# Optimization experiments

Hardware: AMD Instinct MI355X
Metric: run time of the kernel (lower is better)

Reference implementation:

```python
import jax, jax.numpy as jnp
import numpy as np

D = 12  # grid size per axis (self.shape = [12,12,12])
BN_EPS = 1e-5


def _scatter(feats, idx, B):
    # feats: [N, C], idx: [N, 4] = (b, z, y, x). Coords are unique -> .set is exact.
    g = jnp.zeros((B, D, D, D, feats.shape[-1]), feats.dtype)
    return g.at[idx[:, 0], idx[:, 1], idx[:, 2], idx[:, 3]].set(feats)


def _subm_conv_bn_relu(feats, idx, B, W, b, gamma, beta):
    # Submanifold 3x3x3 conv == dense SAME conv on zero-filled grid, restricted
    # to the active sites (inactive neighbors contribute zero features).
    g = _scatter(feats, idx, B)  # [B, D, D, D, Cin]
    y = jax.lax.conv_general_dilated(
        g, W, window_strides=(1, 1, 1), padding='SAME',
        dimension_numbers=('NDHWC', 'DHWIO', 'NDHWC')) + b
    f = y[idx[:, 0], idx[:, 1], idx[:, 2], idx[:, 3]]  # gather active -> [N, Cout]
    # BatchNorm1d (training mode): biased batch stats over the N active points.
    mu = f.mean(axis=0)
    var = f.var(axis=0)
    f = (f - mu) * jax.lax.rsqrt(var + BN_EPS) * gamma + beta
    return jax.nn.relu(f)


def setup_inputs() -> dict:
    key = jax.random.key(0)
    B, per, Cin = 512, 864, 16
    N = B * per
    k_feat, k_coord, kp = jax.random.split(key, 3)
    # unique active voxels per batch element
    pkeys = jax.random.split(k_coord, B)
    lin = jax.vmap(lambda k: jax.random.permutation(k, D * D * D))(pkeys)[:, :per]  # [B, per]
    z, y, x = lin // (D * D), (lin // D) % D, lin % D
    bids = jnp.broadcast_to(jnp.arange(B)[:, None], (B, per))
    indices = jnp.stack([bids, z, y, x], axis=-1).reshape(N, 4).astype(jnp.int32)
    features = jax.random.normal(k_feat, (N, Cin), dtype=jnp.float32)
    ks = jax.random.split(kp, 6)
    inp = {
        'features': features, 'indices': indices, 'batch_size': B,
        'W0': jax.random.normal(ks[0], (3, 3, 3, Cin, 64), jnp.float32) * 0.05,
        'b0': jax.random.normal(ks[1], (64,), jnp.float32) * 0.05,
        'gamma0': jnp.ones((64,), jnp.float32), 'beta0': jnp.zeros((64,), jnp.float32),
        'W1': jax.random.normal(ks[2], (3, 3, 3, 64, 128), jnp.float32) * 0.05,
        'b1': jax.random.normal(ks[3], (128,), jnp.float32) * 0.05,
        'gamma1': jnp.ones((128,), jnp.float32), 'beta1': jnp.zeros((128,), jnp.float32),
        'W2': jax.random.normal(ks[4], (3, 3, 3, 128, 64), jnp.float32) * 0.05,
        'b2': jax.random.normal(ks[5], (64,), jnp.float32) * 0.05,
        'gamma2': jnp.ones((64,), jnp.float32), 'beta2': jnp.zeros((64,), jnp.float32),
    }
    return inp


def reference(features, indices, batch_size, W0, b0, gamma0, beta0,
              W1, b1, gamma1, beta1, W2, b2, gamma2, beta2):
    B = int(batch_size)
    f = _subm_conv_bn_relu(features, indices, B, W0, b0, gamma0, beta0)
    f = _subm_conv_bn_relu(f, indices, B, W1, b1, gamma1, beta1)
    f = _subm_conv_bn_relu(f, indices, B, W2, b2, gamma2, beta2)
    g = _scatter(f, indices, B)                 # [B, D, D, D, Cout]
    return jnp.transpose(g, (0, 4, 1, 2, 3))    # spconv .dense(): [B, C, D, H, W]
```

## Files before the change

kernel.cpp:

```cpp
#include <hip/hip_runtime.h>

#define DD 12
#define VOX 1728
#define BN_EPS 1e-5f
#define BATCH 512
#define PER 864
#define PERZ 865
#define NTOT (BATCH * PER)

typedef __attribute__((ext_vector_type(8))) short short8;
typedef __attribute__((ext_vector_type(4))) float f32x4;
typedef unsigned short u16;

__device__ inline u16 f2b(float f) {
    union { float f; unsigned u; } v; v.f = f;
    unsigned r = v.u + 0x7fffu + ((v.u >> 16) & 1u);
    return (u16)(r >> 16);
}
__device__ inline float b2f(u16 h) {
    union { unsigned u; float f; } v; v.u = ((unsigned)h) << 16;
    return v.f;
}
constexpr int ilog2(int v) { return v == 1 ? 0 : 1 + ilog2(v / 2); }

__device__ __forceinline__ void async_copy16(const void* g, void* l) {
    __builtin_amdgcn_global_load_lds(
        (const __attribute__((address_space(1))) void*)g,
        (__attribute__((address_space(3))) void*)l, 16, 0, 0);
}

template<int N> __device__ __forceinline__ void wait_vm() {
    if constexpr (N == 0)       asm volatile("s_waitcnt vmcnt(0)"  ::: "memory");
    else if constexpr (N == 4)  asm volatile("s_waitcnt vmcnt(4)"  ::: "memory");
    else if constexpr (N == 8)  asm volatile("s_waitcnt vmcnt(8)"  ::: "memory");
    else if constexpr (N == 16) asm volatile("s_waitcnt vmcnt(16)" ::: "memory");
    else static_assert(N == 0, "unhandled vmcnt value");
}

__global__ void build_map_kernel(const int* __restrict__ idx, int* __restrict__ map, int N) {
    int p = blockIdx.x * blockDim.x + threadIdx.x;
    if (p >= N) return;
    const int4 v = ((const int4*)idx)[p];
    map[v.x * VOX + (v.y * DD + v.z) * DD + v.w] = p;
}

__global__ void build_nbr_kernel(const int* __restrict__ idx, const int* __restrict__ map,
                                 u16* __restrict__ nbr, int N) {
    int p = blockIdx.x * blockDim.x + threadIdx.x;
    if (p >= N) return;
    const int4 v = ((const int4*)idx)[p];
    const int base = v.x * VOX;
    const int lb = v.x * PER;
    #pragma unroll
    for (int nk = 0; nk < 27; nk++) {
        int dz = nk / 9 - 1, dy = (nk / 3) % 3 - 1, dx = nk % 3 - 1;
        int zz = v.y + dz, yy = v.z + dy, xx = v.w + dx;
        u16 out = PER;
        if (zz >= 0 && zz < DD && yy >= 0 && yy < DD && xx >= 0 && xx < DD) {
            int q = map[base + (zz * DD + yy) * DD + xx];
            if (q >= 0) out = (u16)(q - lb);
        }
        nbr[nk * N + p] = out;
    }
    #pragma unroll
    for (int nk = 27; nk < 32; nk++) nbr[nk * N + p] = PER;
}

template<int CIN, int COUT>
__global__ void pack_w_kernel(const float* __restrict__ W, u16* __restrict__ Wp) {
    constexpr int K = 27 * CIN;
    constexpr int KSTEPS = ((K + 63) & ~63) / 64;
    constexpr int NG = COUT / 64;
    int t = blockIdx.x * blockDim.x + threadIdx.x;
    if (t >= KSTEPS * NG * 8 * 64) return;
    int lane = t & 63;
    int sj   = (t >> 6) & 7;
    int gg   = t >> 9;
    int g = gg % NG, step = gg / NG;
    int col = g * 64 + (sj & 3) * 16 + (lane & 15);
    int k0  = step * 64 + (sj >> 2) * 32 + (lane >> 4) * 8;
    short8 o;
    #pragma unroll
    for (int e = 0; e < 8; e++) {
        int k = k0 + e;
        u16 val = 0;
        if (k < K) val = f2b(W[(size_t)k * COUT + col]);
        ((u16*)&o)[e] = val;
    }
    *(short8*)(Wp + (size_t)t * 8) = o;
}

__global__ void zero_rows_kernel(u16* __restrict__ f, int CIN) {
    int t = blockIdx.x * blockDim.x + threadIdx.x;
    int e4 = CIN >> 2;
    if (t >= BATCH * e4) return;
    int b = t / e4, k = t - b * e4;
    ((ushort4*)f)[(size_t)(b * PERZ + PER) * e4 + k] = make_ushort4(0, 0, 0, 0);
}

__global__ void cast_bf16_kernel(const float* __restrict__ in, u16* __restrict__ out, int N4) {
    int i = blockIdx.x * blockDim.x + threadIdx.x;
    if (i >= N4) return;
    float4 v = ((const float4*)in)[i];
    int p = i >> 2, c4 = i & 3;
    int b = p / PER, r = p - b * PER;
    ushort4 o;
    o.x = f2b(v.x); o.y = f2b(v.y); o.z = f2b(v.z); o.w = f2b(v.w);
    ((ushort4*)out)[(size_t)(b * PERZ + r) * 4 + c4] = o;
}

template<int CIN, int COUT, int BM, int WM, int WN>
__global__ __launch_bounds__(256) void conv_mfma_kernel(
    const u16* __restrict__ fin,
    const u16* __restrict__ nbr,
    const u16* __restrict__ Wp,
    const float* __restrict__ bias,
    float* __restrict__ y,
    float* __restrict__ stats) {
    constexpr int Kpad   = (27 * CIN + 63) & ~63;
    constexpr int KSTEPS = Kpad / 64;
    constexpr int L2C    = ilog2(CIN);
    constexpr int NG     = COUT / 64;
    constexpr int ASLOTS = BM / 32;
    constexpr int BUFB   = BM * 128;
    static_assert(KSTEPS >= 3, "pipeline prologue needs >=3 K-steps");
    __shared__ char smem[2 * BUFB];

    const int perx = gridDim.x >> 3;
    const int bid = (blockIdx.x & 7) * perx + (blockIdx.x >> 3);
    const int p0 = bid * BM;

    const int tid = threadIdx.x;
    const int wave = tid >> 6, lane = tid & 63;
    const int wm = wave / WN, wn = wave % WN;
    const int lq = lane >> 4, lr = lane & 15;
    const int lrow = lane >> 3;
    const int kc_d = (lane & 7) ^ (lrow & 7);

    const int qv0 = ((((kc_d * 8) >> L2C) * NTOT) + p0 + wave * ASLOTS * 8 + lrow) * 2;
    int gbase[ASLOTS];
    #pragma unroll
    for (int i = 0; i < ASLOTS; i++) {
        int p = p0 + (wave * ASLOTS + i) * 8 + lrow;
        int b = p / PER;
        gbase[i] = b * PERZ * CIN + ((kc_d * 8) & (CIN - 1));
    }

    const int phs0 = ((0 + lq) ^ (lr & 7)) * 16;
    const int phs1 = ((4 + lq) ^ (lr & 7)) * 16;
    const int aBase = (wm * 64 + lr) * 128;

    const f32x4 fzero = {0.f, 0.f, 0.f, 0.f};
    f32x4 acc[4][4];
    #pragma unroll
    for (int i = 0; i < 4; i++)
        #pragma unroll
        for (int j = 0; j < 4; j++) acc[i][j] = fzero;

    u16 q[ASLOTS];
    short8 bb[8];
    auto loadQ = [&](int step) {
        int sQ = qv0 + ((step * 64) >> L2C) * (NTOT * 2);
        #pragma unroll
        for (int i = 0; i < ASLOTS; i++)
            q[i] = *(const u16*)((const char*)nbr + sQ + i * 16);
    };
    auto stage = [&](int step, int bo) {
        int sG = (step * 64) & (CIN - 1);
        const u16* fs = fin + sG;
        #pragma unroll
        for (int i = 0; i < ASLOTS; i++)
            async_copy16(fs + gbase[i] + ((int)q[i] << L2C),
                         smem + bo + (wave * ASLOTS + i) * 1024);
    };
    const char* wpB = (const char*)Wp + (size_t)wn * 8 * 1024 + (size_t)lane * 16;
    auto loadB = [&](int step) {
        const char* src = wpB + (size_t)step * (NG * 8 * 1024);
        #pragma unroll
        for (int sj = 0; sj < 8; sj++)
            bb[sj] = *(const short8*)(src + sj * 1024);
    };
    auto compute = [&](int so) {
        #pragma unroll
        for (int s = 0; s < 2; s++) {
            const int ph = s ? phs1 : phs0;
            short8 af[4];
            #pragma unroll
            for (int i = 0; i < 4; i++)
                af[i] = *(const short8*)(smem + so + aBase + i * 2048 + ph);
            #pragma unroll
            for (int i = 0; i < 4; i++)
                #pragma unroll
                for (int j = 0; j < 4; j++)
                    acc[i][j] = __builtin_amdgcn_mfma_f32_16x16x32_bf16(af[i], bb[s * 4 + j], acc[i][j], 0, 0, 0);
        }
    };

    loadQ(0);
    stage(0, 0);
    loadB(0);
    loadQ(1);

    #pragma unroll 1
    for (int kb = 0; kb < KSTEPS; kb++) {
        if (kb + 1 < KSTEPS) {
            stage(kb + 1, ((kb + 1) & 1) * BUFB);
            if (kb + 2 < KSTEPS) {
                loadQ(kb + 2);
                wait_vm<2 * ASLOTS>();
            } else {
                wait_vm<ASLOTS>();
            }
        } else {
            wait_vm<0>();
        }
        __builtin_amdgcn_s_barrier();

        compute((kb & 1) * BUFB);

        __builtin_amdgcn_sched_barrier(0);
        if (kb + 1 < KSTEPS) loadB(kb + 1);

        asm volatile("s_waitcnt lgkmcnt(0)" ::: "memory");
        __builtin_amdgcn_s_barrier();
    }

    #pragma unroll
    for (int j = 0; j < 4; j++) {
        int col = wn * 64 + j * 16 + lr;
        float bv = bias[col];
        float s = 0.f, s2 = 0.f;
        #pragma unroll
        for (int i = 0; i < 4; i++) {
            int row0 = p0 + wm * 64 + i * 16 + lq * 4;
            #pragma unroll
            for (int r = 0; r < 4; r++) {
                float v = acc[i][j][r] + bv;
                y[(size_t)(row0 + r) * COUT + col] = v;
                s += v; s2 += v * v;
            }
        }
        s  += __shfl_down(s, 32);  s  += __shfl_down(s, 16);
        s2 += __shfl_down(s2, 32); s2 += __shfl_down(s2, 16);
        if (lane < 16) {
            atomicAdd(&stats[col], s);
            atomicAdd(&stats[COUT + col], s2);
        }
    }
}

template<int COUT>
__global__ void finalize_kernel(const float* __restrict__ stats, const float* __restrict__ gamma,
                                const float* __restrict__ beta, float* __restrict__ ss, int N) {
    int co = threadIdx.x;
    float inv_n = 1.f / (float)N;
    float mu  = stats[co] * inv_n;
    float var = stats[COUT + co] * inv_n - mu * mu;
    float sc  = gamma[co] * rsqrtf(var + BN_EPS);
    ss[co]        = sc;
    ss[COUT + co] = beta[co] - mu * sc;
}

template<int COUT>
__global__ void apply_kernel(const float* __restrict__ y, const float* __restrict__ ss,
                             u16* __restrict__ f, int total4) {
    int i = blockIdx.x * blockDim.x + threadIdx.x;
    if (i >= total4) return;
    constexpr int E4 = COUT / 4;
    float4 v = ((const float4*)y)[i];
    int p = i / E4, k = i - p * E4;
    int c0 = k * 4;
    int b = p / PER, r = p - b * PER;
    ushort4 o;
    float a;
    a = fmaf(v.x, ss[c0 + 0], ss[COUT + c0 + 0]); o.x = f2b(a > 0.f ? a : 0.f);
    a = fmaf(v.y, ss[c0 + 1], ss[COUT + c0 + 1]); o.y = f2b(a > 0.f ? a : 0.f);
    a = fmaf(v.z, ss[c0 + 2], ss[COUT + c0 + 2]); o.z = f2b(a > 0.f ? a : 0.f);
    a = fmaf(v.w, ss[c0 + 3], ss[COUT + c0 + 3]); o.w = f2b(a > 0.f ? a : 0.f);
    ((ushort4*)f)[(size_t)(b * PERZ + r) * E4 + k] = o;
}

__global__ void output_kernel(const u16* __restrict__ f, const int* __restrict__ map,
                              float* __restrict__ out, int total) {
    int i = blockIdx.x * blockDim.x + threadIdx.x;
    if (i >= total) return;
    int voxel = i % VOX;
    int bc    = i / VOX;
    int c = bc & 63;
    int b = bc >> 6;
    int p = map[b * VOX + voxel];
    float v = 0.f;
    if (p >= 0) {
        int r = p - b * PER;
        v = b2f(f[(size_t)(b * PERZ + r) * 64 + c]);
    }
    out[i] = v;
}

extern "C" void kernel_launch(void* const* d_in, const int* in_sizes, int n_in,
                              void* d_out, int out_size, void* d_ws, size_t ws_size,
                              hipStream_t stream) {
    const float* feats = (const float*)d_in[0];
    const int*   idx   = (const int*)  d_in[1];
    const float* W0 = (const float*)d_in[3];
    const float* b0 = (const float*)d_in[4];
    const float* g0 = (const float*)d_in[5];
    const float* e0 = (const float*)d_in[6];
    const float* W1 = (const float*)d_in[7];
    const float* b1 = (const float*)d_in[8];
    const float* g1 = (const float*)d_in[9];
    const float* e1 = (const float*)d_in[10];
    const float* W2 = (const float*)d_in[11];
    const float* b2 = (const float*)d_in[12];
    const float* g2 = (const float*)d_in[13];
    const float* e2 = (const float*)d_in[14];

    const int N = in_sizes[0] / 16;

    char* ws = (char*)d_ws;
    size_t off = 0;
    auto alloc = [&](size_t bytes) { void* p = ws + off; off = (off + bytes + 255) & ~(size_t)255; return p; };
    int*   map   = (int*)  alloc((size_t)BATCH * VOX * 4);
    float* stats = (float*)alloc(3 * 256 * 4);
    float* ss    = (float*)alloc(3 * 256 * 4);
    u16*   nbr   = (u16*)  alloc((size_t)N * 32 * 2);
    u16*   wt0   = (u16*)  alloc((size_t)7  * 1 * 512 * 16);
    u16*   wt1   = (u16*)  alloc((size_t)27 * 2 * 512 * 16);
    u16*   wt2   = (u16*)  alloc((size_t)54 * 1 * 512 * 16);
    u16*   fbuf  = (u16*)  alloc((size_t)BATCH * PERZ * 128 * 2);
    float* y = (float*)d_out;

    hipMemsetAsync(map,   0xFF, (size_t)BATCH * VOX * 4, stream);
    hipMemsetAsync(stats, 0,    3 * 256 * 4, stream);
    build_map_kernel<<<(N + 255) / 256, 256, 0, stream>>>(idx, map, N);
    build_nbr_kernel<<<(N + 255) / 256, 256, 0, stream>>>(idx, map, nbr, N);
    pack_w_kernel<16,  64 ><<<(7  * 1 * 512 + 255) / 256, 256, 0, stream>>>(W0, wt0);
    pack_w_kernel<64,  128><<<(27 * 2 * 512 + 255) / 256, 256, 0, stream>>>(W1, wt1);
    pack_w_kernel<128, 64 ><<<(54 * 1 * 512 + 255) / 256, 256, 0, stream>>>(W2, wt2);

    zero_rows_kernel<<<(BATCH * 4 + 255) / 256, 256, 0, stream>>>(fbuf, 16);
    cast_bf16_kernel<<<(N * 4 + 255) / 256, 256, 0, stream>>>(feats, fbuf, N * 4);
    conv_mfma_kernel<16, 64, 256, 4, 1><<<N / 256, 256, 0, stream>>>(fbuf, nbr, wt0, b0, y, stats + 0);
    finalize_kernel<64><<<1, 64, 0, stream>>>(stats + 0, g0, e0, ss + 0, N);
    zero_rows_kernel<<<(BATCH * 16 + 255) / 256, 256, 0, stream>>>(fbuf, 64);
    apply_kernel<64><<<(N * 16 + 255) / 256, 256, 0, stream>>>(y, ss + 0, fbuf, N * 16);

    conv_mfma_kernel<64, 128, 128, 2, 2><<<N / 128, 256, 0, stream>>>(fbuf, nbr, wt1, b1, y, stats + 256);
    finalize_kernel<128><<<1, 128, 0, stream>>>(stats + 256, g1, e1, ss + 256, N);
    zero_rows_kernel<<<(BATCH * 32 + 255) / 256, 256, 0, stream>>>(fbuf, 128);
    apply_kernel<128><<<(N * 32 + 255) / 256, 256, 0, stream>>>(y, ss + 256, fbuf, N * 32);

    conv_mfma_kernel<128, 64, 256, 4, 1><<<N / 256, 256, 0, stream>>>(fbuf, nbr, wt2, b2, y, stats + 512);
    finalize_kernel<64><<<1, 64, 0, stream>>>(stats + 512, g2, e2, ss + 512, N);
    zero_rows_kernel<<<(BATCH * 16 + 255) / 256, 256, 0, stream>>>(fbuf, 64);
    apply_kernel<64><<<(N * 16 + 255) / 256, 256, 0, stream>>>(y, ss + 512, fbuf, N * 16);

    output_kernel<<<(out_size + 255) / 256, 256, 0, stream>>>(fbuf, map, (float*)d_out, out_size);
}
```

Baseline: 1.407 ms.

## Fuse final BN-apply with dense scatter and restructure conv pipeline waits

Replaces the last layer's apply, zero-rows and output kernels with one fused kernel. It reads the fp32 conv output from a new workspace buffer, applies the BN scale and shift plus ReLU, and writes the channel-major dense output through an LDS transpose. This removes a bf16 round trip and a scattered-gather output pass. It also reworks the conv main loop's synchronisation: one vmcnt(0) wait and barrier at the top, the trailing lgkmcnt wait and barrier dropped, and a shallower prefetch schedule for the CIN=128 layer. Dropping the trailing barrier risks LDS races between loadB and the next stage, and the fused path only runs if the workspace is large enough.

After: 1.401 ms. Within noise of the previous version (-0.4%).

```diff
diff --git a/kernel.cpp b/kernel.cpp
--- a/kernel.cpp
+++ b/kernel.cpp
@@ -29,12 +29,8 @@
         (__attribute__((address_space(3))) void*)l, 16, 0, 0);
 }
 
-template<int N> __device__ __forceinline__ void wait_vm() {
-    if constexpr (N == 0)       asm volatile("s_waitcnt vmcnt(0)"  ::: "memory");
-    else if constexpr (N == 4)  asm volatile("s_waitcnt vmcnt(4)"  ::: "memory");
-    else if constexpr (N == 8)  asm volatile("s_waitcnt vmcnt(8)"  ::: "memory");
-    else if constexpr (N == 16) asm volatile("s_waitcnt vmcnt(16)" ::: "memory");
-    else static_assert(N == 0, "unhandled vmcnt value");
+__device__ __forceinline__ void wait_vm0() {
+    asm volatile("s_waitcnt vmcnt(0)" ::: "memory");
 }
 
 __global__ void build_map_kernel(const int* __restrict__ idx, int* __restrict__ map, int N) {
@@ -199,30 +195,24 @@
     loadQ(0);
     stage(0, 0);
     loadB(0);
-    loadQ(1);
+    if constexpr (CIN != 128) loadQ(1);
 
     #pragma unroll 1
     for (int kb = 0; kb < KSTEPS; kb++) {
-        if (kb + 1 < KSTEPS) {
+        wait_vm0();
+        __builtin_amdgcn_s_barrier();
+        __builtin_amdgcn_sched_barrier(0);
+        if (kb + 1 < KSTEPS)
             stage(kb + 1, ((kb + 1) & 1) * BUFB);
-            if (kb + 2 < KSTEPS) {
-                loadQ(kb + 2);
-                wait_vm<2 * ASLOTS>();
-            } else {
-                wait_vm<ASLOTS>();
-            }
+        if constexpr (CIN == 128) {
+            if (!(kb & 1) && kb + 2 < KSTEPS) loadQ(kb + 2);
         } else {
-            wait_vm<0>();
-        }
-        __builtin_amdgcn_s_barrier();
-
+            if (kb + 2 < KSTEPS) loadQ(kb + 2);
+        }
+        __builtin_amdgcn_sched_barrier(0);
         compute((kb & 1) * BUFB);
-
         __builtin_amdgcn_sched_barrier(0);
         if (kb + 1 < KSTEPS) loadB(kb + 1);
-
-        asm volatile("s_waitcnt lgkmcnt(0)" ::: "memory");
-        __builtin_amdgcn_s_barrier();
     }
 
     #pragma unroll
@@ -297,6 +287,34 @@
     out[i] = v;
 }
 
+__global__ void output_fused_kernel(const float* __restrict__ y, const float* __restrict__ ss,
+                                    const int* __restrict__ map, float* __restrict__ out) {
+    __shared__ float tile[64][65];
+    __shared__ int   prow[64];
+    const int chunk = blockIdx.x;
+    const int b  = chunk / (VOX / 64);
+    const int v0 = (chunk % (VOX / 64)) * 64;
+    const int t = threadIdx.x;
+    if (t < 64) prow[t] = map[b * VOX + v0 + t];
+    __syncthreads();
+    const int c = t & 63;
+    const float sc = ss[c], sh = ss[64 + c];
+    for (int v = t >> 6; v < 64; v += 4) {
+        int p = prow[v];
+        float val = 0.f;
+        if (p >= 0) {
+            float a = fmaf(y[(size_t)p * 64 + c], sc, sh);
+            val = a > 0.f ? a : 0.f;
+        }
+        tile[v][c] = val;
+    }
+    __syncthreads();
+    const int vv = t & 63;
+    #pragma unroll
+    for (int cc = t >> 6; cc < 64; cc += 4)
+        out[(size_t)(b * 64 + cc) * VOX + v0 + vv] = tile[vv][cc];
+}
+
 extern "C" void kernel_launch(void* const* d_in, const int* in_sizes, int n_in,
                               void* d_out, int out_size, void* d_ws, size_t ws_size,
                               hipStream_t stream) {
@@ -330,6 +348,10 @@
     u16*   fbuf  = (u16*)  alloc((size_t)BATCH * PERZ * 128 * 2);
     float* y = (float*)d_out;
 
+    const size_t y3_bytes = (size_t)N * 64 * 4;
+    float* y3 = nullptr;
+    if (off + y3_bytes <= ws_size) y3 = (float*)alloc(y3_bytes);
+
     hipMemsetAsync(map,   0xFF, (size_t)BATCH * VOX * 4, stream);
     hipMemsetAsync(stats, 0,    3 * 256 * 4, stream);
     build_map_kernel<<<(N + 255) / 256, 256, 0, stream>>>(idx, map, N);
@@ -350,10 +372,15 @@
     zero_rows_kernel<<<(BATCH * 32 + 255) / 256, 256, 0, stream>>>(fbuf, 128);
     apply_kernel<128><<<(N * 32 + 255) / 256, 256, 0, stream>>>(y, ss + 256, fbuf, N * 32);
 
-    conv_mfma_kernel<128, 64, 256, 4, 1><<<N / 256, 256, 0, stream>>>(fbuf, nbr, wt2, b2, y, stats + 512);
+    float* yL3 = y3 ? y3 : y;
+    conv_mfma_kernel<128, 64, 256, 4, 1><<<N / 256, 256, 0, stream>>>(fbuf, nbr, wt2, b2, yL3, stats + 512);
     finalize_kernel<64><<<1, 64, 0, stream>>>(stats + 512, g2, e2, ss + 512, N);
-    zero_rows_kernel<<<(BATCH * 16 + 255) / 256, 256, 0, stream>>>(fbuf, 64);
-    apply_kernel<64><<<(N * 16 + 255) / 256, 256, 0, stream>>>(y, ss + 512, fbuf, N * 16);
-
-    output_kernel<<<(out_size + 255) / 256, 256, 0, stream>>>(fbuf, map, (float*)d_out, out_size);
-}
+
+    if (y3) {
+        output_fused_kernel<<<BATCH * (VOX / 64), 256, 0, stream>>>(y3, ss + 512, map, (float*)d_out);
+    } else {
+        zero_rows_kernel<<<(BATCH * 16 + 255) / 256, 256, 0, stream>>>(fbuf, 64);
+        apply_kernel<64><<<(N * 16 + 255) / 256, 256, 0, stream>>>(y, ss + 512, fbuf, N * 16);
+        output_kernel<<<(out_size + 255) / 256, 256, 0, stream>>>(fbuf, map, (float*)d_out, out_size);
+    }
+}
```
